# Optimization experiments

Measured on AMD Instinct MI355X. Metric: run time of the kernel, lower is better.

## Reference

```python
import jax, jax.numpy as jnp
from jax import lax
import numpy as np

# ---- geometry constants (from metadata / module __init__) ----
NA = 1152            # rotview (number of projection angles)
ND = 736             # det_count
NP = 512             # reconstructed image size
VOX = 1.0 / 0.7      # vox_scaling
D   = VOX * 595.0    # source-to-isocenter distance
DD  = VOX * 490.6    # isocenter-to-detector distance
DU  = VOX * 1.2858   # detector pixel spacing
DSD = D + DD         # source-to-detector distance
ANGLES = np.linspace(0.0, 2.0 * np.pi, NA, endpoint=False) + np.pi / 2.0

# ---- Shepp-Logan Fourier filter (skimage/torch-radon construction) ----
PAD = max(64, int(2 ** np.ceil(np.log2(2 * ND))))  # 2048

def _shepp_logan_filter(size):
    n = np.concatenate([np.arange(1, size // 2 + 1, 2),
                        np.arange(size // 2 - 1, 0, -2)])
    f = np.zeros(size)
    f[0] = 0.25
    f[1::2] = -1.0 / (np.pi * n) ** 2
    four = 2.0 * np.real(np.fft.fft(f))            # ramp filter
    omega = np.pi * np.fft.fftfreq(size)[1:]
    four[1:] *= np.sin(omega) / omega              # Shepp-Logan window
    return four[: size // 2 + 1].astype(np.float32)  # rfft half-spectrum

FILT = jnp.asarray(_shepp_logan_filter(PAD))
COS_A = jnp.asarray(np.cos(ANGLES).astype(np.float32))
SIN_A = jnp.asarray(np.sin(ANGLES).astype(np.float32))


def _filter_sinogram(sino):
    # sino: (NA, ND). Zero-pad to PAD, filter in Fourier domain, crop.
    padded = jnp.pad(sino, ((0, 0), (0, PAD - ND)))
    spec = jnp.fft.rfft(padded, axis=-1) * FILT
    filt = jnp.fft.irfft(spec, n=PAD, axis=-1)[:, :ND]
    return filt * (np.pi / (2.0 * NA))


def _backproject(filtered):
    # Pixel-driven fan-beam (flat detector) backprojection.
    c = (NP - 1) / 2.0
    coords = jnp.arange(NP, dtype=jnp.float32) - c
    ys, xs = jnp.meshgrid(coords, coords, indexing='ij')  # (NP, NP)

    def body(acc, inp):
        cb, sb, row = inp
        pdot = xs * cb + ys * sb            # pixel coord along source dir
        pe = -xs * sb + ys * cb             # pixel coord along detector axis
        den = D - pdot                      # source->pixel depth
        u = DSD * pe / den                  # detector coordinate (mm)
        iu = u / DU + (ND - 1) / 2.0        # fractional detector index
        i0 = jnp.floor(iu)
        frac = iu - i0
        i0i = i0.astype(jnp.int32)
        valid = (i0i >= 0) & (i0i < ND - 1) & (den > 0)
        i0c = jnp.clip(i0i, 0, ND - 2)
        v = row[i0c] * (1.0 - frac) + row[i0c + 1] * frac  # linear interp
        w = (D / den) ** 2                   # fan-beam distance weighting
        return acc + jnp.where(valid, w * v, 0.0), None

    img, _ = lax.scan(body, jnp.zeros((NP, NP), jnp.float32),
                      (COS_A, SIN_A, filtered))
    return img


def setup_inputs() -> dict:
    key = jax.random.key(0)
    x = jax.random.normal(key, (1, 1, NA, ND), dtype=jnp.float32)
    return {"x": x}


def reference(x):
    sino = x[0, 0]                          # (NA, ND) after squeeze
    filtered = _filter_sinogram(sino)
    fbp = _backproject(filtered)
    # mu -> HU -> normalize to [0, 1] window
    fbp_hu = (1000.0 * ((fbp - 0.0192) / 0.0192) - (-1024.0)) / (3072.0 - (-1024.0))
    return fbp_hu[None, None]               # (1, 1, 512, 512)
```

## Files before the change

### kernel.cpp

```cpp
#include <hip/hip_runtime.h>
#include <math.h>

#ifndef M_PI
#define M_PI 3.14159265358979323846
#endif

#define NAANG 1152
#define NDET  736
#define NPIX  512
#define PADN  2048
#define NHALF 1025

#define OFF_COST  0
#define OFF_FILTF 8192
#define OFF_H     12416
#define OFF_TRIG  20608
#define OFF_FS    39040
#define OFF_PART  3430528

typedef float f32x2 __attribute__((ext_vector_type(2)));

static __device__ __forceinline__ f32x2 load2(const float* p) {
    f32x2 r;
    __builtin_memcpy(&r, p, 8);
    return r;
}

__global__ void costab_kernel(float* __restrict__ cosT) {
    int r = blockIdx.x * 256 + threadIdx.x;
    cosT[r] = (float)cos(2.0 * M_PI * (double)r / (double)PADN);
}

__global__ void filt_spec_kernel(const float* __restrict__ cosT,
                                 float* __restrict__ filt_f) {
    __shared__ float red[256];
    const int m = blockIdx.x;
    const int t = threadIdx.x;
    float s = 0.f;
    for (int j = t; j < 1024; j += 256) {
        int n = (j < 512) ? (2 * j + 1) : (2047 - 2 * j);
        float fj = (float)(-1.0 / ((M_PI * n) * (M_PI * n)));
        s += fj * cosT[(m * (2 * j + 1)) & (PADN - 1)];
    }
    red[t] = s;
    __syncthreads();
    for (int w = 128; w > 0; w >>= 1) {
        if (t < w) red[t] += red[t + w];
        __syncthreads();
    }
    if (t == 0) {
        double four = 2.0 * (0.25 + (double)red[0]);
        if (m > 0) {
            double om = M_PI * (double)m / (double)PADN;
            four *= sin(om) / om;
        }
        filt_f[m] = (float)four;
    }
}

__global__ void h_kernel(const float* __restrict__ cosT,
                         const float* __restrict__ filt_f,
                         float* __restrict__ h, float4* __restrict__ trig) {
    __shared__ float red[256];
    const int k = blockIdx.x;
    const int t = threadIdx.x;
    if (t == 0 && k < NAANG) {
        double ang = 2.0 * M_PI * (double)k / (double)NAANG + M_PI / 2.0;
        double c = cos(ang), s = sin(ang);
        double K = 1085.6 / 1.2858;
        trig[k] = make_float4((float)c, (float)s, (float)(K * c), (float)(K * s));
    }
    float s = 0.f;
    for (int m = t; m <= 1024; m += 256) {
        float F = filt_f[m];
        float c;
        if (m == 0) c = 1.f;
        else if (m == 1024) c = (k & 1) ? -1.f : 1.f;
        else c = 2.f * cosT[(m * k) & (PADN - 1)];
        s += F * c;
    }
    red[t] = s;
    __syncthreads();
    for (int w = 128; w > 0; w >>= 1) {
        if (t < w) red[t] += red[t + w];
        __syncthreads();
    }
    if (t == 0)
        h[k] = (float)((double)red[0] / (double)PADN * (M_PI / (2.0 * (double)NAANG)));
}

__global__ void conv_kernel(const float* __restrict__ x,
                            const float* __restrict__ h,
                            float* __restrict__ fs) {
    __shared__ float sh2[2816];
    __shared__ float srow[NDET];
    const int row = blockIdx.x;
    const int t = threadIdx.x;
    const float4* h4 = (const float4*)h;
    for (int i = t; i < 704; i += 192) ((float4*)sh2)[i] = h4[i & 511];
    const float4* x4 = (const float4*)(x + row * NDET);
    for (int i = t; i < NDET / 4; i += 192) ((float4*)srow)[i] = x4[i];
    __syncthreads();

    const int t4 = 4 * t;
    float o0 = 0.f, o1 = 0.f, o2 = 0.f, o3 = 0.f;
    #pragma unroll 2
    for (int j = 0; j < NDET; j += 4) {
        float4 r4 = *(const float4*)&srow[j];
        const int A = t4 + PADN - j;
        float4 hlo = *(const float4*)&sh2[A - 4];
        float4 hhi = *(const float4*)&sh2[A];
        o0 = fmaf(r4.x, hhi.x, o0); o0 = fmaf(r4.y, hlo.w, o0);
        o0 = fmaf(r4.z, hlo.z, o0); o0 = fmaf(r4.w, hlo.y, o0);
        o1 = fmaf(r4.x, hhi.y, o1); o1 = fmaf(r4.y, hhi.x, o1);
        o1 = fmaf(r4.z, hlo.w, o1); o1 = fmaf(r4.w, hlo.z, o1);
        o2 = fmaf(r4.x, hhi.z, o2); o2 = fmaf(r4.y, hhi.y, o2);
        o2 = fmaf(r4.z, hhi.x, o2); o2 = fmaf(r4.w, hlo.w, o2);
        o3 = fmaf(r4.x, hhi.w, o3); o3 = fmaf(r4.y, hhi.z, o3);
        o3 = fmaf(r4.z, hhi.y, o3); o3 = fmaf(r4.w, hhi.x, o3);
    }
    if (t < NDET / 4)
        *(float4*)&fs[row * NDET + t4] = make_float4(o0, o1, o2, o3);
}

#define GEO(AA, G0,G1,G2,G3, FR0,FR1,FR2,FR3, W0,W1,W2,W3)               \
  {                                                                      \
    float4 q = trig[abase + (AA)];           \
    float den0 = fmaf(-xs, q.x, fmaf(-ys0, q.y, Dg));                    \
    float kpe0 = fmaf(ys0, q.z, -(xs * q.w));                            \
    float sb2 = q.y + q.y, kc2 = q.z + q.z;                              \
    float den1 = den0 - q.y, den2 = den0 - sb2, den3 = den2 - q.y;       \
    float kpe1 = kpe0 + q.z, kpe2 = kpe0 + kc2, kpe3 = kpe2 + q.z;       \
    float r0 = __builtin_amdgcn_rcpf(den0);                              \
    float r1 = __builtin_amdgcn_rcpf(den1);                              \
    float r2 = __builtin_amdgcn_rcpf(den2);                              \
    float r3 = __builtin_amdgcn_rcpf(den3);                              \
    float iu0 = fmaf(kpe0, r0, 367.5f);                                  \
    float iu1 = fmaf(kpe1, r1, 367.5f);                                  \
    float iu2 = fmaf(kpe2, r2, 367.5f);                                  \
    float iu3 = fmaf(kpe3, r3, 367.5f);                                  \
    float f0 = floorf(iu0), f1 = floorf(iu1);                            \
    float f2 = floorf(iu2), f3 = floorf(iu3);                            \
    int i0 = (int)f0, i1 = (int)f1, i2 = (int)f2, i3 = (int)f3;          \
    int c0 = min(max(i0, 0), NDET - 2);                                  \
    int c1 = min(max(i1, 0), NDET - 2);                                  \
    int c2 = min(max(i2, 0), NDET - 2);                                  \
    int c3 = min(max(i3, 0), NDET - 2);                                  \
    const float* rp = fs + (size_t)(abase + (AA)) * NDET;                \
    G0 = load2(rp + c0); G1 = load2(rp + c1);                            \
    G2 = load2(rp + c2); G3 = load2(rp + c3);                            \
    FR0 = iu0 - f0; FR1 = iu1 - f1; FR2 = iu2 - f2; FR3 = iu3 - f3;      \
    float d0 = Dg * r0, d1 = Dg * r1, d2 = Dg * r2, d3 = Dg * r3;        \
    W0 = ((unsigned)i0 < (unsigned)(NDET - 1)) ? d0 * d0 : 0.f;          \
    W1 = ((unsigned)i1 < (unsigned)(NDET - 1)) ? d1 * d1 : 0.f;          \
    W2 = ((unsigned)i2 < (unsigned)(NDET - 1)) ? d2 * d2 : 0.f;          \
    W3 = ((unsigned)i3 < (unsigned)(NDET - 1)) ? d3 * d3 : 0.f;          \
  }

#define CONSUME(G0,G1,G2,G3, FR0,FR1,FR2,FR3, W0,W1,W2,W3)               \
  {                                                                      \
    float v0 = fmaf(FR0, G0.y - G0.x, G0.x);                             \
    float v1 = fmaf(FR1, G1.y - G1.x, G1.x);                             \
    float v2 = fmaf(FR2, G2.y - G2.x, G2.x);                             \
    float v3 = fmaf(FR3, G3.y - G3.x, G3.x);                             \
    acc0 = fmaf(W0, v0, acc0); acc1 = fmaf(W1, v1, acc1);                \
    acc2 = fmaf(W2, v2, acc2); acc3 = fmaf(W3, v3, acc3);                \
  }

template<int NCH>
__global__ __launch_bounds__(256, 8)
void backproj_kernel(const float* __restrict__ fs,
                     const float4* __restrict__ trig,
                     float* __restrict__ partial) {
    constexpr int ACL = NAANG / NCH;
    const int t = threadIdx.x;
    const int abase = blockIdx.z * ACL;
    const int ix = blockIdx.x * 256 + t;
    const int iy = blockIdx.y * 4;
    const float xs  = (float)ix - 255.5f;
    const float ys0 = (float)iy - 255.5f;
    const float Dg = 850.0f;

    float acc0 = 0.f, acc1 = 0.f, acc2 = 0.f, acc3 = 0.f;
    f32x2 Ag0, Ag1, Ag2, Ag3, Bg0, Bg1, Bg2, Bg3;
    float Af0, Af1, Af2, Af3, Aw0, Aw1, Aw2, Aw3;
    float Bf0, Bf1, Bf2, Bf3, Bw0, Bw1, Bw2, Bw3;

    GEO(0, Ag0,Ag1,Ag2,Ag3, Af0,Af1,Af2,Af3, Aw0,Aw1,Aw2,Aw3);
    int a = 0;
    for (; a + 2 < ACL; a += 2) {
        GEO(a + 1, Bg0,Bg1,Bg2,Bg3, Bf0,Bf1,Bf2,Bf3, Bw0,Bw1,Bw2,Bw3);
        CONSUME(Ag0,Ag1,Ag2,Ag3, Af0,Af1,Af2,Af3, Aw0,Aw1,Aw2,Aw3);
        GEO(a + 2, Ag0,Ag1,Ag2,Ag3, Af0,Af1,Af2,Af3, Aw0,Aw1,Aw2,Aw3);
        CONSUME(Bg0,Bg1,Bg2,Bg3, Bf0,Bf1,Bf2,Bf3, Bw0,Bw1,Bw2,Bw3);
    }
    GEO(ACL - 1, Bg0,Bg1,Bg2,Bg3, Bf0,Bf1,Bf2,Bf3, Bw0,Bw1,Bw2,Bw3);
    CONSUME(Ag0,Ag1,Ag2,Ag3, Af0,Af1,Af2,Af3, Aw0,Aw1,Aw2,Aw3);
    CONSUME(Bg0,Bg1,Bg2,Bg3, Bf0,Bf1,Bf2,Bf3, Bw0,Bw1,Bw2,Bw3);

    float* outp = partial + ((size_t)blockIdx.z * NPIX + iy) * NPIX + ix;
    outp[0 * NPIX] = acc0;
    outp[1 * NPIX] = acc1;
    outp[2 * NPIX] = acc2;
    outp[3 * NPIX] = acc3;
}

template<int NCH>
__global__ void combine_kernel(const float* __restrict__ partial,
                               float* __restrict__ out) {
    int p = blockIdx.x * 256 + threadIdx.x;
    float s = 0.f;
    #pragma unroll
    for (int c = 0; c < NCH; ++c) s += partial[c * NPIX * NPIX + p];
    out[p] = fmaf(s, (float)(1000.0 / 0.0192 / 4096.0), 0.005859375f);
}

extern "C" void kernel_launch(void* const* d_in, const int* in_sizes, int n_in,
                              void* d_out, int out_size, void* d_ws, size_t ws_size,
                              hipStream_t stream) {
    const float* x = (const float*)d_in[0];
    float* out = (float*)d_out;

    char* ws = (char*)d_ws;
    float*  cosT   = (float*)(ws + OFF_COST);
    float*  filt_f = (float*)(ws + OFF_FILTF);
    float*  h      = (float*)(ws + OFF_H);
    float4* trig   = (float4*)(ws + OFF_TRIG);
    float*  fs     = (float*)(ws + OFF_FS);
    float*  part   = (float*)(ws + OFF_PART);

    costab_kernel<<<PADN / 256, 256, 0, stream>>>(cosT);
    filt_spec_kernel<<<NHALF, 256, 0, stream>>>(cosT, filt_f);
    h_kernel<<<PADN, 256, 0, stream>>>(cosT, filt_f, h, trig);
    conv_kernel<<<NAANG, 192, 0, stream>>>(x, h, fs);

    const size_t pbytes = (size_t)NPIX * NPIX * 4;
    if (ws_size >= OFF_PART + 8 * pbytes) {
        backproj_kernel<8><<<dim3(2, 128, 8), 256, 0, stream>>>(fs, trig, part);
        combine_kernel<8><<<NPIX * NPIX / 256, 256, 0, stream>>>(part, out);
    } else if (ws_size >= OFF_PART + 4 * pbytes) {
        backproj_kernel<4><<<dim3(2, 128, 4), 256, 0, stream>>>(fs, trig, part);
        combine_kernel<4><<<NPIX * NPIX / 256, 256, 0, stream>>>(part, out);
    } else if (ws_size >= OFF_PART + 2 * pbytes) {
        backproj_kernel<2><<<dim3(2, 128, 2), 256, 0, stream>>>(fs, trig, part);
        combine_kernel<2><<<NPIX * NPIX / 256, 256, 0, stream>>>(part, out);
    } else {
        backproj_kernel<1><<<dim3(2, 128, 1), 256, 0, stream>>>(fs, trig, part);
        combine_kernel<1><<<NPIX * NPIX / 256, 256, 0, stream>>>(part, out);
    }
}
```

Measured before the change: 264.3 us.

## Tile backprojection into 2D blocks, widen convolution, drop cosine table kernel

Backprojection threads now cover 32x32 pixel tiles (16x16 per wave) rather than 256-wide row strips. Neighbouring threads therefore hit nearby detector samples, which should improve cache locality of the gathers. The trig table loads are software-prefetched one angle ahead, and the D^2 weight scaling is folded into the final combine constant. The convolution now handles two rows per block with 8 outputs per thread to reuse shared-memory loads. The cosine lookup table kernel is replaced by inline cospif calls, which may slightly change precision of the filter setup.

```diff
diff --git a/kernel.cpp b/kernel.cpp
--- a/kernel.cpp
+++ b/kernel.cpp
@@ -11,12 +11,11 @@
 #define PADN  2048
 #define NHALF 1025
 
-#define OFF_COST  0
-#define OFF_FILTF 8192
-#define OFF_H     12416
-#define OFF_TRIG  20608
-#define OFF_FS    39040
-#define OFF_PART  3430528
+#define OFF_FILTF 0
+#define OFF_H     4224
+#define OFF_TRIG  12416
+#define OFF_FS    30848
+#define OFF_PART  3422336
 
 typedef float f32x2 __attribute__((ext_vector_type(2)));
 
@@ -26,13 +25,7 @@
     return r;
 }
 
-__global__ void costab_kernel(float* __restrict__ cosT) {
-    int r = blockIdx.x * 256 + threadIdx.x;
-    cosT[r] = (float)cos(2.0 * M_PI * (double)r / (double)PADN);
-}
-
-__global__ void filt_spec_kernel(const float* __restrict__ cosT,
-                                 float* __restrict__ filt_f) {
+__global__ void filt_spec_kernel(float* __restrict__ filt_f) {
     __shared__ float red[256];
     const int m = blockIdx.x;
     const int t = threadIdx.x;
@@ -40,7 +33,8 @@
     for (int j = t; j < 1024; j += 256) {
         int n = (j < 512) ? (2 * j + 1) : (2047 - 2 * j);
         float fj = (float)(-1.0 / ((M_PI * n) * (M_PI * n)));
-        s += fj * cosT[(m * (2 * j + 1)) & (PADN - 1)];
+        int r = (m * (2 * j + 1)) & (PADN - 1);
+        s += fj * cospif((float)r * (1.0f / 1024.0f));
     }
     red[t] = s;
     __syncthreads();
@@ -58,8 +52,7 @@
     }
 }
 
-__global__ void h_kernel(const float* __restrict__ cosT,
-                         const float* __restrict__ filt_f,
+__global__ void h_kernel(const float* __restrict__ filt_f,
                          float* __restrict__ h, float4* __restrict__ trig) {
     __shared__ float red[256];
     const int k = blockIdx.x;
@@ -76,7 +69,7 @@
         float c;
         if (m == 0) c = 1.f;
         else if (m == 1024) c = (k & 1) ? -1.f : 1.f;
-        else c = 2.f * cosT[(m * k) & (PADN - 1)];
+        else c = 2.f * cospif((float)((m * k) & (PADN - 1)) * (1.0f / 1024.0f));
         s += F * c;
     }
     red[t] = s;
@@ -93,44 +86,54 @@
                             const float* __restrict__ h,
                             float* __restrict__ fs) {
     __shared__ float sh2[2816];
-    __shared__ float srow[NDET];
-    const int row = blockIdx.x;
-    const int t = threadIdx.x;
+    __shared__ float srow[2][NDET];
+    const int t = threadIdx.x;
+    const int row0 = blockIdx.x * 2;
     const float4* h4 = (const float4*)h;
     for (int i = t; i < 704; i += 192) ((float4*)sh2)[i] = h4[i & 511];
-    const float4* x4 = (const float4*)(x + row * NDET);
-    for (int i = t; i < NDET / 4; i += 192) ((float4*)srow)[i] = x4[i];
+    const float4* x4 = (const float4*)(x + (size_t)row0 * NDET);
+    for (int i = t; i < 368; i += 192) ((float4*)srow[0])[i] = x4[i];
     __syncthreads();
 
-    const int t4 = 4 * t;
-    float o0 = 0.f, o1 = 0.f, o2 = 0.f, o3 = 0.f;
+    const int r = t / 96;
+    const int u = t % 96;
+    const float* my = srow[r];
+    const int A0 = 8 * u + PADN;
+    float o[8] = {0.f, 0.f, 0.f, 0.f, 0.f, 0.f, 0.f, 0.f};
     #pragma unroll 2
-    for (int j = 0; j < NDET; j += 4) {
-        float4 r4 = *(const float4*)&srow[j];
-        const int A = t4 + PADN - j;
-        float4 hlo = *(const float4*)&sh2[A - 4];
-        float4 hhi = *(const float4*)&sh2[A];
-        o0 = fmaf(r4.x, hhi.x, o0); o0 = fmaf(r4.y, hlo.w, o0);
-        o0 = fmaf(r4.z, hlo.z, o0); o0 = fmaf(r4.w, hlo.y, o0);
-        o1 = fmaf(r4.x, hhi.y, o1); o1 = fmaf(r4.y, hhi.x, o1);
-        o1 = fmaf(r4.z, hlo.w, o1); o1 = fmaf(r4.w, hlo.z, o1);
-        o2 = fmaf(r4.x, hhi.z, o2); o2 = fmaf(r4.y, hhi.y, o2);
-        o2 = fmaf(r4.z, hhi.x, o2); o2 = fmaf(r4.w, hlo.w, o2);
-        o3 = fmaf(r4.x, hhi.w, o3); o3 = fmaf(r4.y, hhi.z, o3);
-        o3 = fmaf(r4.z, hhi.y, o3); o3 = fmaf(r4.w, hhi.x, o3);
-    }
-    if (t < NDET / 4)
-        *(float4*)&fs[row * NDET + t4] = make_float4(o0, o1, o2, o3);
-}
-
-#define GEO(AA, G0,G1,G2,G3, FR0,FR1,FR2,FR3, W0,W1,W2,W3)               \
+    for (int j = 0; j < NDET; j += 8) {
+        float4 s0 = *(const float4*)&my[j];
+        float4 s1 = *(const float4*)&my[j + 4];
+        const float* hp = &sh2[A0 - j - 8];
+        float4 h0 = *(const float4*)(hp);
+        float4 h1 = *(const float4*)(hp + 4);
+        float4 h2 = *(const float4*)(hp + 8);
+        float4 h3 = *(const float4*)(hp + 12);
+        float wv[16] = {h0.x, h0.y, h0.z, h0.w, h1.x, h1.y, h1.z, h1.w,
+                        h2.x, h2.y, h2.z, h2.w, h3.x, h3.y, h3.z, h3.w};
+        float se[8]  = {s0.x, s0.y, s0.z, s0.w, s1.x, s1.y, s1.z, s1.w};
+        #pragma unroll
+        for (int e = 0; e < 8; ++e) {
+            #pragma unroll
+            for (int d = 0; d < 8; ++d)
+                o[d] = fmaf(se[e], wv[8 + d - e], o[d]);
+        }
+    }
+    if (u < 92) {
+        float* op = fs + (size_t)(row0 + r) * NDET + 8 * u;
+        *(float4*)op       = make_float4(o[0], o[1], o[2], o[3]);
+        *(float4*)(op + 4) = make_float4(o[4], o[5], o[6], o[7]);
+    }
+}
+
+#define GEO(AA, QQ, G0,G1,G2,G3, FR0,FR1,FR2,FR3, W0,W1,W2,W3)           \
   {                                                                      \
-    float4 q = trig[abase + (AA)];           \
-    float den0 = fmaf(-xs, q.x, fmaf(-ys0, q.y, Dg));                    \
-    float kpe0 = fmaf(ys0, q.z, -(xs * q.w));                            \
-    float sb2 = q.y + q.y, kc2 = q.z + q.z;                              \
-    float den1 = den0 - q.y, den2 = den0 - sb2, den3 = den2 - q.y;       \
-    float kpe1 = kpe0 + q.z, kpe2 = kpe0 + kc2, kpe3 = kpe2 + q.z;       \
+    const float* rp = fs + (size_t)(abase + (AA)) * NDET;                \
+    float den0 = fmaf(-xs, QQ.x, fmaf(-ys0, QQ.y, Dg));                  \
+    float kpe0 = fmaf(ys0, QQ.z, -(xs * QQ.w));                          \
+    float sb2 = QQ.y + QQ.y, kc2 = QQ.z + QQ.z;                          \
+    float den1 = den0 - QQ.y, den2 = den0 - sb2, den3 = den2 - QQ.y;     \
+    float kpe1 = kpe0 + QQ.z, kpe2 = kpe0 + kc2, kpe3 = kpe2 + QQ.z;     \
     float r0 = __builtin_amdgcn_rcpf(den0);                              \
     float r1 = __builtin_amdgcn_rcpf(den1);                              \
     float r2 = __builtin_amdgcn_rcpf(den2);                              \
@@ -146,15 +149,13 @@
     int c1 = min(max(i1, 0), NDET - 2);                                  \
     int c2 = min(max(i2, 0), NDET - 2);                                  \
     int c3 = min(max(i3, 0), NDET - 2);                                  \
-    const float* rp = fs + (size_t)(abase + (AA)) * NDET;                \
     G0 = load2(rp + c0); G1 = load2(rp + c1);                            \
     G2 = load2(rp + c2); G3 = load2(rp + c3);                            \
     FR0 = iu0 - f0; FR1 = iu1 - f1; FR2 = iu2 - f2; FR3 = iu3 - f3;      \
-    float d0 = Dg * r0, d1 = Dg * r1, d2 = Dg * r2, d3 = Dg * r3;        \
-    W0 = ((unsigned)i0 < (unsigned)(NDET - 1)) ? d0 * d0 : 0.f;          \
-    W1 = ((unsigned)i1 < (unsigned)(NDET - 1)) ? d1 * d1 : 0.f;          \
-    W2 = ((unsigned)i2 < (unsigned)(NDET - 1)) ? d2 * d2 : 0.f;          \
-    W3 = ((unsigned)i3 < (unsigned)(NDET - 1)) ? d3 * d3 : 0.f;          \
+    W0 = ((unsigned)i0 < (unsigned)(NDET - 1)) ? r0 * r0 : 0.f;          \
+    W1 = ((unsigned)i1 < (unsigned)(NDET - 1)) ? r1 * r1 : 0.f;          \
+    W2 = ((unsigned)i2 < (unsigned)(NDET - 1)) ? r2 * r2 : 0.f;          \
+    W3 = ((unsigned)i3 < (unsigned)(NDET - 1)) ? r3 * r3 : 0.f;          \
   }
 
 #define CONSUME(G0,G1,G2,G3, FR0,FR1,FR2,FR3, W0,W1,W2,W3)               \
@@ -174,11 +175,14 @@
                      float* __restrict__ partial) {
     constexpr int ACL = NAANG / NCH;
     const int t = threadIdx.x;
+    const int lane = t & 63, wave = t >> 6;
+    const int lx = lane & 15, lq = lane >> 4;
+    const int wx = wave & 1,  wy = wave >> 1;
+    const int X = blockIdx.x * 32 + wx * 16 + lx;
+    const int Y = blockIdx.y * 32 + wy * 16 + lq * 4;
     const int abase = blockIdx.z * ACL;
-    const int ix = blockIdx.x * 256 + t;
-    const int iy = blockIdx.y * 4;
-    const float xs  = (float)ix - 255.5f;
-    const float ys0 = (float)iy - 255.5f;
+    const float xs  = (float)X - 255.5f;
+    const float ys0 = (float)Y - 255.5f;
     const float Dg = 850.0f;
 
     float acc0 = 0.f, acc1 = 0.f, acc2 = 0.f, acc3 = 0.f;
@@ -186,19 +190,23 @@
     float Af0, Af1, Af2, Af3, Aw0, Aw1, Aw2, Aw3;
     float Bf0, Bf1, Bf2, Bf3, Bw0, Bw1, Bw2, Bw3;
 
-    GEO(0, Ag0,Ag1,Ag2,Ag3, Af0,Af1,Af2,Af3, Aw0,Aw1,Aw2,Aw3);
+    float4 qc = trig[abase];
+    float4 qn = trig[abase + 1];
+    GEO(0, qc, Ag0,Ag1,Ag2,Ag3, Af0,Af1,Af2,Af3, Aw0,Aw1,Aw2,Aw3);
     int a = 0;
     for (; a + 2 < ACL; a += 2) {
-        GEO(a + 1, Bg0,Bg1,Bg2,Bg3, Bf0,Bf1,Bf2,Bf3, Bw0,Bw1,Bw2,Bw3);
+        float4 q2 = trig[abase + a + 2];
+        GEO(a + 1, qn, Bg0,Bg1,Bg2,Bg3, Bf0,Bf1,Bf2,Bf3, Bw0,Bw1,Bw2,Bw3);
         CONSUME(Ag0,Ag1,Ag2,Ag3, Af0,Af1,Af2,Af3, Aw0,Aw1,Aw2,Aw3);
-        GEO(a + 2, Ag0,Ag1,Ag2,Ag3, Af0,Af1,Af2,Af3, Aw0,Aw1,Aw2,Aw3);
+        qn = trig[abase + a + 3];
+        GEO(a + 2, q2, Ag0,Ag1,Ag2,Ag3, Af0,Af1,Af2,Af3, Aw0,Aw1,Aw2,Aw3);
         CONSUME(Bg0,Bg1,Bg2,Bg3, Bf0,Bf1,Bf2,Bf3, Bw0,Bw1,Bw2,Bw3);
     }
-    GEO(ACL - 1, Bg0,Bg1,Bg2,Bg3, Bf0,Bf1,Bf2,Bf3, Bw0,Bw1,Bw2,Bw3);
+    GEO(ACL - 1, qn, Bg0,Bg1,Bg2,Bg3, Bf0,Bf1,Bf2,Bf3, Bw0,Bw1,Bw2,Bw3);
     CONSUME(Ag0,Ag1,Ag2,Ag3, Af0,Af1,Af2,Af3, Aw0,Aw1,Aw2,Aw3);
     CONSUME(Bg0,Bg1,Bg2,Bg3, Bf0,Bf1,Bf2,Bf3, Bw0,Bw1,Bw2,Bw3);
 
-    float* outp = partial + ((size_t)blockIdx.z * NPIX + iy) * NPIX + ix;
+    float* outp = partial + ((size_t)blockIdx.z * NPIX + Y) * NPIX + X;
     outp[0 * NPIX] = acc0;
     outp[1 * NPIX] = acc1;
     outp[2 * NPIX] = acc2;
@@ -212,7 +220,8 @@
     float s = 0.f;
     #pragma unroll
     for (int c = 0; c < NCH; ++c) s += partial[c * NPIX * NPIX + p];
-    out[p] = fmaf(s, (float)(1000.0 / 0.0192 / 4096.0), 0.005859375f);
+    const float scale = (float)(722500.0 * 1000.0 / 0.0192 / 4096.0);
+    out[p] = fmaf(s, scale, 0.005859375f);
 }
 
 extern "C" void kernel_launch(void* const* d_in, const int* in_sizes, int n_in,
@@ -222,30 +231,28 @@
     float* out = (float*)d_out;
 
     char* ws = (char*)d_ws;
-    float*  cosT   = (float*)(ws + OFF_COST);
     float*  filt_f = (float*)(ws + OFF_FILTF);
     float*  h      = (float*)(ws + OFF_H);
     float4* trig   = (float4*)(ws + OFF_TRIG);
     float*  fs     = (float*)(ws + OFF_FS);
     float*  part   = (float*)(ws + OFF_PART);
 
-    costab_kernel<<<PADN / 256, 256, 0, stream>>>(cosT);
-    filt_spec_kernel<<<NHALF, 256, 0, stream>>>(cosT, filt_f);
-    h_kernel<<<PADN, 256, 0, stream>>>(cosT, filt_f, h, trig);
-    conv_kernel<<<NAANG, 192, 0, stream>>>(x, h, fs);
+    filt_spec_kernel<<<NHALF, 256, 0, stream>>>(filt_f);
+    h_kernel<<<PADN, 256, 0, stream>>>(filt_f, h, trig);
+    conv_kernel<<<NAANG / 2, 192, 0, stream>>>(x, h, fs);
 
     const size_t pbytes = (size_t)NPIX * NPIX * 4;
     if (ws_size >= OFF_PART + 8 * pbytes) {
-        backproj_kernel<8><<<dim3(2, 128, 8), 256, 0, stream>>>(fs, trig, part);
+        backproj_kernel<8><<<dim3(16, 16, 8), 256, 0, stream>>>(fs, trig, part);
         combine_kernel<8><<<NPIX * NPIX / 256, 256, 0, stream>>>(part, out);
     } else if (ws_size >= OFF_PART + 4 * pbytes) {
-        backproj_kernel<4><<<dim3(2, 128, 4), 256, 0, stream>>>(fs, trig, part);
+        backproj_kernel<4><<<dim3(16, 16, 4), 256, 0, stream>>>(fs, trig, part);
         combine_kernel<4><<<NPIX * NPIX / 256, 256, 0, stream>>>(part, out);
     } else if (ws_size >= OFF_PART + 2 * pbytes) {
-        backproj_kernel<2><<<dim3(2, 128, 2), 256, 0, stream>>>(fs, trig, part);
+        backproj_kernel<2><<<dim3(16, 16, 2), 256, 0, stream>>>(fs, trig, part);
         combine_kernel<2><<<NPIX * NPIX / 256, 256, 0, stream>>>(part, out);
     } else {
-        backproj_kernel<1><<<dim3(2, 128, 1), 256, 0, stream>>>(fs, trig, part);
+        backproj_kernel<1><<<dim3(16, 16, 1), 256, 0, stream>>>(fs, trig, part);
         combine_kernel<1><<<NPIX * NPIX / 256, 256, 0, stream>>>(part, out);
     }
 }
```

After: 269.4 us. About the same (+1.9%).
